# Optimization experiments

Measured on AMD Instinct MI355X. Metric: run time of the kernel, lower is better.

The kernel has to match this reference:

```python
import jax, jax.numpy as jnp
import numpy as np

B, S, D, K = 4, 2048, 1024, 8

def setup_inputs() -> dict:
    key = jax.random.key(0)
    k1, k2, k3 = jax.random.split(key, 3)
    hidden_states = jax.random.normal(k1, (B, S, D), dtype=jnp.float32)
    # scaled so scores ~ O(1) and exp() does not overflow
    W_phi = jax.random.normal(k2, (D, D), dtype=jnp.float32) * 0.005
    W_psi = jax.random.normal(k3, (D, D), dtype=jnp.float32) * 0.005
    return {"hidden_states": hidden_states, "W_phi": W_phi, "W_psi": W_psi, "k": K}

def reference(hidden_states, W_phi, W_psi, k):
    b, s, d = hidden_states.shape
    k = min(k, s)
    # nn.Linear(bias=False): y = x @ W.T
    phi_h = hidden_states @ W_phi.T            # [b,s,d]
    psi_h = hidden_states @ W_psi.T            # [b,s,d]
    scores = jnp.einsum('bsd,btd->bst', phi_h, psi_h)  # [b,s,s]
    affinity = jnp.exp(scores)
    topk_values, topk_indices = jax.lax.top_k(affinity, k)   # [b,s,k]
    norm_sum = topk_values.sum(axis=-1, keepdims=True) + 1e-8
    normalized_weights = topk_values / norm_sum
    batch_offset = (jnp.arange(b) * s)[:, None, None]        # [b,1,1]
    src_local = jnp.arange(s)[None, :, None]                 # [1,s,1]
    src_global = jnp.broadcast_to(batch_offset + src_local, (b, s, k))
    dst_global = batch_offset + topk_indices
    mask = (topk_indices != src_local).reshape(-1)           # drop self-loops
    # eager boolean compaction (data-dependent size, like the torch module)
    src_final = src_global.reshape(-1)[mask]
    dst_final = dst_global.reshape(-1)[mask]
    weights_final = normalized_weights.reshape(-1)[mask]
    if src_final.size == 0:
        all_nodes = jnp.arange(b * s)
        return jnp.stack([all_nodes, all_nodes], axis=0), jnp.ones(b * s, dtype=jnp.float32)
    edge_index = jnp.stack([src_final, dst_final], axis=0)
    return edge_index, weights_final
```

## Files before the change

kernel.cpp:

```cpp
#include <hip/hip_runtime.h>
#include <cmath>

#define SEQ 2048
#define DDIM 1024
#define NROWS 8192
#define KSEL 8
#define NCAND 12
#define IMAXC 0x7fffffff

typedef __attribute__((ext_vector_type(8))) short bf16x8;
typedef __attribute__((ext_vector_type(4))) float f32x4;
typedef __attribute__((ext_vector_type(4))) double f64x4;

__device__ __forceinline__ unsigned short f2bf(float f) {
  unsigned u = __builtin_bit_cast(unsigned, f);
  u = (u + 0x7fffu + ((u >> 16) & 1u)) >> 16;
  return (unsigned short)u;
}
__device__ __forceinline__ float bf2f(unsigned short h) {
  unsigned u = ((unsigned)h) << 16;
  return __builtin_bit_cast(float, u);
}
__device__ __forceinline__ unsigned pkbf(float a, float b) {
  unsigned r;
  asm("v_cvt_pk_bf16_f32 %0, %1, %2" : "=v"(r) : "v"(a), "v"(b));
  return r;
}
__device__ __forceinline__ void dmap(int sel, int lg, int lr, int rg,
                                     int& ri, int& ci) {
  switch (sel) {
    case 0:  ri = (lg << 2) + rg; ci = lr; break;
    case 1:  ri = lg + (rg << 2); ci = lr; break;
    case 2:  ri = lr; ci = (lg << 2) + rg; break;
    default: ri = lr; ci = lg + (rg << 2); break;
  }
}

__global__ void kprobe(int* __restrict__ sel) {
  const int lane = threadIdx.x;
  const int lr = lane & 15, lg = lane >> 4;
  const double a = (double)(4 * lr + lg + 1);
  const double b = (double)(9 * lr + 5 * lg + 2);
  f64x4 d = (f64x4){0.0, 0.0, 0.0, 0.0};
  d = __builtin_amdgcn_mfma_f64_16x16x4f64(a, b, d, 0, 0, 0);
  int my = 4;
  for (int s = 3; s >= 0; --s) {
    bool ok = true;
    for (int rg = 0; rg < 4; ++rg) {
      int ri, ci;
      dmap(s, lg, lr, rg, ri, ci);
      double e = 0.0;
      for (int k = 0; k < 4; ++k)
        e += (double)(4 * ri + k + 1) * (double)(9 * ci + 5 * k + 2);
      ok = ok && (d[rg] == e);
    }
    if (__all(ok)) my = s;
  }
  if (lane == 0) sel[0] = my;
}

#define K0_STAGE(bi)                                        \
  do {                                                      \
    *reinterpret_cast<float4*>(&As[bi][kr][c4]) = pa0;      \
    *reinterpret_cast<float4*>(&As[bi][kr][c4 + 32]) = pa1; \
    *reinterpret_cast<float4*>(&Bs[bi][kr][c4]) = pb0;      \
    *reinterpret_cast<float4*>(&Bs[bi][kr][c4 + 32]) = pb1; \
  } while (0)

__global__ __launch_bounds__(256, 2)
void k0_mfma(const float* __restrict__ A, const float* __restrict__ B,
             float* __restrict__ C, const int* __restrict__ selp) {
  const int sel = selp[0];
  if (sel >= 4) return;
  __shared__ float As[2][32][72];
  __shared__ float Bs[2][32][72];
  const int tid = threadIdx.x;
  const int lane = tid & 63, w = tid >> 6;
  const int wr = w >> 1, wc = w & 1;
  const int lr = lane & 15, lg = lane >> 4;
  const int brow = blockIdx.y << 6, bcol = blockIdx.x << 6;
  const int kr = tid >> 3, c4 = (tid & 7) << 2;

  f64x4 acc[2][2];
#pragma unroll
  for (int mi = 0; mi < 2; ++mi)
#pragma unroll
    for (int nj = 0; nj < 2; ++nj)
      acc[mi][nj] = (f64x4){0.0, 0.0, 0.0, 0.0};

  const float* Ap = &A[(size_t)kr * DDIM + brow + c4];
  const float* Bp = &B[(size_t)kr * DDIM + bcol + c4];
  float4 pa0 = *reinterpret_cast<const float4*>(Ap);
  float4 pa1 = *reinterpret_cast<const float4*>(Ap + 32);
  float4 pb0 = *reinterpret_cast<const float4*>(Bp);
  float4 pb1 = *reinterpret_cast<const float4*>(Bp + 32);
  K0_STAGE(0);
  {
    const size_t nk = (size_t)32 * DDIM;
    pa0 = *reinterpret_cast<const float4*>(Ap + nk);
    pa1 = *reinterpret_cast<const float4*>(Ap + nk + 32);
    pb0 = *reinterpret_cast<const float4*>(Bp + nk);
    pb1 = *reinterpret_cast<const float4*>(Bp + nk + 32);
  }

  for (int t = 0; t < 32; ++t) {
    __syncthreads();
    const int cur = t & 1;
    if (t < 31) {
      K0_STAGE(cur ^ 1);
      if (t < 30) {
        const size_t nk = (size_t)(t + 2) * 32 * DDIM;
        pa0 = *reinterpret_cast<const float4*>(Ap + nk);
        pa1 = *reinterpret_cast<const float4*>(Ap + nk + 32);
        pb0 = *reinterpret_cast<const float4*>(Bp + nk);
        pb1 = *reinterpret_cast<const float4*>(Bp + nk + 32);
      }
    }
    __builtin_amdgcn_s_setprio(1);
#pragma unroll
    for (int kp = 0; kp < 8; ++kp) {
      const int ka = (kp << 2) + lg;
      double a[2], b[2];
#pragma unroll
      for (int mi = 0; mi < 2; ++mi)
        a[mi] = (double)As[cur][ka][(wr << 5) + (mi << 4) + lr];
#pragma unroll
      for (int nj = 0; nj < 2; ++nj)
        b[nj] = (double)Bs[cur][ka][(wc << 5) + (nj << 4) + lr];
#pragma unroll
      for (int mi = 0; mi < 2; ++mi)
#pragma unroll
        for (int nj = 0; nj < 2; ++nj)
          acc[mi][nj] = __builtin_amdgcn_mfma_f64_16x16x4f64(
              a[mi], b[nj], acc[mi][nj], 0, 0, 0);
    }
    __builtin_amdgcn_s_setprio(0);
  }
#pragma unroll
  for (int mi = 0; mi < 2; ++mi)
#pragma unroll
    for (int nj = 0; nj < 2; ++nj)
#pragma unroll
      for (int rg = 0; rg < 4; ++rg) {
        int ri, ci;
        dmap(sel, lg, lr, rg, ri, ci);
        C[(size_t)(brow + (wr << 5) + (mi << 4) + ri) * DDIM +
          bcol + (wc << 5) + (nj << 4) + ci] = (float)acc[mi][nj][rg];
      }
}

__global__ __launch_bounds__(256)
void k0_repair(const float* __restrict__ A, const float* __restrict__ B,
               float* __restrict__ C, const int* __restrict__ selp) {
  if (selp[0] < 4) return;
  __shared__ __align__(16) float As[32][68];
  __shared__ __align__(16) float Bs[32][68];
  const int tid = threadIdx.x;
  const int tx = tid & 15, ty = tid >> 4;
  const int brow = blockIdx.y << 6;
  const int bcol = blockIdx.x << 6;
  double acc[4][4] = {};
  for (int k0 = 0; k0 < DDIM; k0 += 32) {
#pragma unroll
    for (int i = 0; i < 2; ++i) {
      const int f = tid + (i << 8);
      const int r = f >> 4;
      const int c4 = (f & 15) << 2;
      *reinterpret_cast<float4*>(&As[r][c4]) =
          *reinterpret_cast<const float4*>(&A[(size_t)(k0 + r) * DDIM + brow + c4]);
      *reinterpret_cast<float4*>(&Bs[r][c4]) =
          *reinterpret_cast<const float4*>(&B[(size_t)(k0 + r) * DDIM + bcol + c4]);
    }
    __syncthreads();
#pragma unroll
    for (int kk = 0; kk < 32; ++kk) {
      const float4 a = *reinterpret_cast<const float4*>(&As[kk][ty << 2]);
      const float4 b = *reinterpret_cast<const float4*>(&Bs[kk][tx << 2]);
      const double ad[4] = {a.x, a.y, a.z, a.w};
      const double bd[4] = {b.x, b.y, b.z, b.w};
#pragma unroll
      for (int i = 0; i < 4; ++i)
#pragma unroll
        for (int j = 0; j < 4; ++j)
          acc[i][j] = fma(ad[i], bd[j], acc[i][j]);
    }
    __syncthreads();
  }
#pragma unroll
  for (int i = 0; i < 4; ++i) {
    float4 v = make_float4((float)acc[i][0], (float)acc[i][1],
                           (float)acc[i][2], (float)acc[i][3]);
    *reinterpret_cast<float4*>(
        &C[(size_t)(brow + (ty << 2) + i) * DDIM + bcol + (tx << 2)]) = v;
  }
}

#define K1_STAGE(bi)                                                \
  do {                                                              \
    As[bi][akh + 0][ar] = pa0.x;  As[bi][akh + 1][ar] = pa0.y;      \
    As[bi][akh + 2][ar] = pa0.z;  As[bi][akh + 3][ar] = pa0.w;      \
    As[bi][akh + 4][ar] = pa1.x;  As[bi][akh + 5][ar] = pa1.y;      \
    As[bi][akh + 6][ar] = pa1.z;  As[bi][akh + 7][ar] = pa1.w;      \
    As[bi][akh + 16][ar] = pa2.x; As[bi][akh + 17][ar] = pa2.y;     \
    As[bi][akh + 18][ar] = pa2.z; As[bi][akh + 19][ar] = pa2.w;     \
    As[bi][akh + 20][ar] = pa3.x; As[bi][akh + 21][ar] = pa3.y;     \
    As[bi][akh + 22][ar] = pa3.z; As[bi][akh + 23][ar] = pa3.w;     \
    *reinterpret_cast<float4*>(&Bs[bi][bk][bc4]) = pb0;             \
    *reinterpret_cast<float4*>(&Bs[bi][bk][bc4 + 64]) = pb1;        \
    *reinterpret_cast<float4*>(&Bs[bi][bk + 16][bc4]) = pb2;        \
    *reinterpret_cast<float4*>(&Bs[bi][bk + 16][bc4 + 64]) = pb3;   \
  } while (0)

#define K1_LOAD(koff)                                                        \
  do {                                                                       \
    pa0 = *reinterpret_cast<const float4*>(Ap + (koff));                     \
    pa1 = *reinterpret_cast<const float4*>(Ap + (koff) + 4);                 \
    pa2 = *reinterpret_cast<const float4*>(Ap + (koff) + 16);                \
    pa3 = *reinterpret_cast<const float4*>(Ap + (koff) + 20);                \
    pb0 = *reinterpret_cast<const float4*>(Bp + (size_t)(koff) * DDIM);      \
    pb1 = *reinterpret_cast<const float4*>(Bp + (size_t)(koff) * DDIM + 64); \
    pb2 = *reinterpret_cast<const float4*>(Bp + (size_t)((koff) + 16) * DDIM);      \
    pb3 = *reinterpret_cast<const float4*>(Bp + (size_t)((koff) + 16) * DDIM + 64); \
  } while (0)

__global__ __launch_bounds__(256, 2)
void k1_mfma(const float* __restrict__ A, const float* __restrict__ B,
             float* __restrict__ C, const int* __restrict__ selp) {
  const int sel = selp[0];
  if (sel >= 4) return;
  __shared__ float As[2][32][144];
  __shared__ float Bs[2][32][144];
  const int tid = threadIdx.x;
  const int lin = blockIdx.y * 8 + blockIdx.x;
  const int nlin = (lin & 7) * 64 + (lin >> 3);
  const int brow = (nlin >> 3) << 7;
  const int bcol = (nlin & 7) << 7;
  const int lane = tid & 63, w = tid >> 6;
  const int wr = w >> 1, wc = w & 1;
  const int lr = lane & 15, lg = lane >> 4;
  const int ar = tid >> 1, akh = (tid & 1) << 3;
  const int bk = tid >> 4, bc4 = (tid & 15) << 2;

  f64x4 acc[4][4];
#pragma unroll
  for (int mi = 0; mi < 4; ++mi)
#pragma unroll
    for (int nj = 0; nj < 4; ++nj)
      acc[mi][nj] = (f64x4){0.0, 0.0, 0.0, 0.0};

  const float* Ap = &A[(size_t)(brow + ar) * DDIM + akh];
  const float* Bp = &B[(size_t)bk * DDIM + bcol + bc4];

  float4 pa0, pa1, pa2, pa3, pb0, pb1, pb2, pb3;
  K1_LOAD(0);
  K1_STAGE(0);
  K1_LOAD(32);

  for (int t = 0; t < 32; ++t) {
    __syncthreads();
    const int cur = t & 1;
    if (t < 31) {
      K1_STAGE(cur ^ 1);
      if (t < 30) K1_LOAD((size_t)(t + 2) << 5);
    }
    __builtin_amdgcn_s_setprio(1);
#pragma unroll
    for (int kp = 0; kp < 8; ++kp) {
      const int ka = (kp << 2) + lg;
      double a[4], b[4];
#pragma unroll
      for (int mi = 0; mi < 4; ++mi)
        a[mi] = (double)As[cur][ka][(wr << 6) + (mi << 4) + lr];
#pragma unroll
      for (int nj = 0; nj < 4; ++nj)
        b[nj] = (double)Bs[cur][ka][(wc << 6) + (nj << 4) + lr];
#pragma unroll
      for (int mi = 0; mi < 4; ++mi)
#pragma unroll
        for (int nj = 0; nj < 4; ++nj)
          acc[mi][nj] = __builtin_amdgcn_mfma_f64_16x16x4f64(
              a[mi], b[nj], acc[mi][nj], 0, 0, 0);
    }
    __builtin_amdgcn_s_setprio(0);
  }
#pragma unroll
  for (int mi = 0; mi < 4; ++mi)
#pragma unroll
    for (int nj = 0; nj < 4; ++nj)
#pragma unroll
      for (int rg = 0; rg < 4; ++rg) {
        int ri, ci;
        dmap(sel, lg, lr, rg, ri, ci);
        C[(size_t)(brow + (wr << 6) + (mi << 4) + ri) * DDIM +
          bcol + (wc << 6) + (nj << 4) + ci] = (float)acc[mi][nj][rg];
      }
}

__global__ __launch_bounds__(256, 2)
void k1_repair(const float* __restrict__ A, const float* __restrict__ B,
               float* __restrict__ C, const int* __restrict__ selp) {
  if (selp[0] < 4) return;
  __shared__ double As[128][17];
  __shared__ double Bs[16][130];
  const int tid = threadIdx.x;
  const int lin = blockIdx.y * 8 + blockIdx.x;
  const int nlin = (lin & 7) * 64 + (lin >> 3);
  const int brow = (nlin >> 3) << 7;
  const int bcol = (nlin & 7) << 7;
  const int tx = tid & 15, ty = tid >> 4;
  const int ar = tid >> 1, aks = (tid & 1) << 3;
  const int bk = tid >> 4, btx = tid & 15;

  double acc[8][8];
#pragma unroll
  for (int i = 0; i < 8; ++i)
#pragma unroll
    for (int j = 0; j < 8; ++j) acc[i][j] = 0.0;

  const float* Aptr = &A[(size_t)(brow + ar) * DDIM + aks];
  const float* Bptr = &B[(size_t)bk * DDIM + bcol + (btx << 1)];

  float4 pa0, pa1;
  float2 pb[4];
  pa0 = *reinterpret_cast<const float4*>(Aptr);
  pa1 = *reinterpret_cast<const float4*>(Aptr + 4);
#pragma unroll
  for (int w = 0; w < 4; ++w)
    pb[w] = *reinterpret_cast<const float2*>(Bptr + (w << 5));

  for (int k0 = 0; k0 < DDIM; k0 += 16) {
    __syncthreads();
    As[ar][aks + 0] = (double)pa0.x; As[ar][aks + 1] = (double)pa0.y;
    As[ar][aks + 2] = (double)pa0.z; As[ar][aks + 3] = (double)pa0.w;
    As[ar][aks + 4] = (double)pa1.x; As[ar][aks + 5] = (double)pa1.y;
    As[ar][aks + 6] = (double)pa1.z; As[ar][aks + 7] = (double)pa1.w;
#pragma unroll
    for (int w = 0; w < 4; ++w) {
      Bs[bk][(btx << 1) + (w << 5) + 0] = (double)pb[w].x;
      Bs[bk][(btx << 1) + (w << 5) + 1] = (double)pb[w].y;
    }
    __syncthreads();
    if (k0 + 16 < DDIM) {
      pa0 = *reinterpret_cast<const float4*>(Aptr + k0 + 16);
      pa1 = *reinterpret_cast<const float4*>(Aptr + k0 + 20);
#pragma unroll
      for (int w = 0; w < 4; ++w)
        pb[w] = *reinterpret_cast<const float2*>(
            Bptr + (size_t)(k0 + 16) * DDIM + (w << 5));
    }
#pragma unroll 8
    for (int kk = 0; kk < 16; ++kk) {
      double a[8];
      double2 b[4];
#pragma unroll
      for (int i = 0; i < 8; ++i) a[i] = As[(ty << 3) + i][kk];
#pragma unroll
      for (int jj = 0; jj < 4; ++jj)
        b[jj] = *reinterpret_cast<const double2*>(&Bs[kk][(tx << 1) + (jj << 5)]);
#pragma unroll
      for (int i = 0; i < 8; ++i) {
#pragma unroll
        for (int jj = 0; jj < 4; ++jj) {
          acc[i][(jj << 1) + 0] = fma(a[i], b[jj].x, acc[i][(jj << 1) + 0]);
          acc[i][(jj << 1) + 1] = fma(a[i], b[jj].y, acc[i][(jj << 1) + 1]);
        }
      }
    }
  }
#pragma unroll
  for (int i = 0; i < 8; ++i) {
    float* crow = &C[(size_t)(brow + (ty << 3) + i) * DDIM + bcol + (tx << 1)];
#pragma unroll
    for (int jj = 0; jj < 4; ++jj) {
      float2 v = make_float2((float)acc[i][(jj << 1)],
                             (float)acc[i][(jj << 1) + 1]);
      *reinterpret_cast<float2*>(crow + (jj << 5)) = v;
    }
  }
}

#define K2_LOAD(koff)                                                         \
  do {                                                                        \
    _Pragma("unroll")                                                         \
    for (int q = 0; q < 4; ++q) {                                             \
      const int c = (q << 9) + tid;                                           \
      const int row = c >> 3;                                                 \
      const int gs = (c & 7) ^ (row & 7);                                     \
      const float* sT = &T[(size_t)(row0g + row) * DDIM + (koff) + (gs << 3)];\
      rT[2 * q] = *reinterpret_cast<const float4*>(sT);                       \
      rT[2 * q + 1] = *reinterpret_cast<const float4*>(sT + 4);               \
      const float* sH = &H[(size_t)(col0g + row) * DDIM + (koff) + (gs << 3)];\
      rH[2 * q] = *reinterpret_cast<const float4*>(sH);                       \
      rH[2 * q + 1] = *reinterpret_cast<const float4*>(sH + 4);               \
    }                                                                         \
  } while (0)

#define K2_STAGE(bi)                                                          \
  do {                                                                        \
    _Pragma("unroll")                                                         \
    for (int q = 0; q < 4; ++q) {                                             \
      const int c = (q << 9) + tid;                                           \
      uint4 o;                                                                \
      o.x = pkbf(rT[2 * q].x, rT[2 * q].y);                                   \
      o.y = pkbf(rT[2 * q].z, rT[2 * q].w);                                   \
      o.z = pkbf(rT[2 * q + 1].x, rT[2 * q + 1].y);                           \
      o.w = pkbf(rT[2 * q + 1].z, rT[2 * q + 1].w);                           \
      *reinterpret_cast<uint4*>(&u.stage[bi][0][c << 3]) = o;                 \
      uint4 o2;                                                               \
      o2.x = pkbf(rH[2 * q].x, rH[2 * q].y);                                  \
      o2.y = pkbf(rH[2 * q].z, rH[2 * q].w);                                  \
      o2.z = pkbf(rH[2 * q + 1].x, rH[2 * q + 1].y);                          \
      o2.w = pkbf(rH[2 * q + 1].z, rH[2 * q + 1].w);                          \
      *reinterpret_cast<uint4*>(&u.stage[bi][1][c << 3]) = o2;                \
    }                                                                         \
  } while (0)

__global__ __launch_bounds__(512, 1)
void k2_mfma(const float* __restrict__ T, const float* __restrict__ H,
             unsigned short* __restrict__ cand_v,
             unsigned char* __restrict__ cand_i) {
  __shared__ union {
    unsigned short stage[2][2][256 * 64];
    float Sl[64][264];
    struct {
      float mv[512][8];
      unsigned char mi[512][8];
    } mg;
  } u;
  const int tid = threadIdx.x;
  const int lane = tid & 63;
  const int w = tid >> 6;
  const int wr = w >> 2, wc = w & 3;
  const int lr = lane & 15, lg = lane >> 4;
  const int lin = blockIdx.z * 64 + blockIdx.y * 8 + blockIdx.x;
  const int nl = (lin & 7) * 32 + (lin >> 3);
  const int bx = nl & 7;
  const int by = (nl >> 3) & 7;
  const int z = nl >> 6;
  const int brow = by << 8, bcol = bx << 8;
  const int row0g = z * SEQ + brow;
  const int col0g = z * SEQ + bcol;

  f32x4 acc[8][4];
#pragma unroll
  for (int mi = 0; mi < 8; ++mi)
#pragma unroll
    for (int nj = 0; nj < 4; ++nj)
      acc[mi][nj] = (f32x4){0.f, 0.f, 0.f, 0.f};

  float4 rT[8], rH[8];
  K2_LOAD(0);
  K2_STAGE(0);
  K2_LOAD(64);

  for (int t = 0; t < 16; ++t) {
    __syncthreads();
    const int cur = t & 1;
    if (t < 15) {
      K2_STAGE(cur ^ 1);
      if (t < 14) K2_LOAD((t + 2) << 6);
    }
#pragma unroll
    for (int kh2 = 0; kh2 < 2; ++kh2) {
      const int sl = (kh2 << 2) + lg;
      bf16x8 bfv[4];
#pragma unroll
      for (int nj = 0; nj < 4; ++nj) {
        const int rb = (wc << 6) + (nj << 4) + lr;
        bfv[nj] = *reinterpret_cast<const bf16x8*>(
            &u.stage[cur][1][(rb << 6) + ((sl ^ (rb & 7)) << 3)]);
      }
#pragma unroll
      for (int mi = 0; mi < 8; ++mi) {
        const int ra = (wr << 7) + (mi << 4) + lr;
        const bf16x8 af = *reinterpret_cast<const bf16x8*>(
            &u.stage[cur][0][(ra << 6) + ((sl ^ (ra & 7)) << 3)]);
#pragma unroll
        for (int nj = 0; nj < 4; ++nj)
          acc[mi][nj] = __builtin_amdgcn_mfma_f32_16x16x32_bf16(
              af, bfv[nj], acc[mi][nj], 0, 0, 0);
      }
    }
  }

  const int srow = tid >> 3;
  const int qd = tid & 7;
#pragma unroll
  for (int p = 0; p < 4; ++p) {
    __syncthreads();
    if (wr == (p >> 1)) {
      const int mib = (p & 1) << 2;
#pragma unroll
      for (int mi2 = 0; mi2 < 4; ++mi2)
#pragma unroll
        for (int nj = 0; nj < 4; ++nj)
#pragma unroll
          for (int rg = 0; rg < 4; ++rg)
            u.Sl[(mi2 << 4) + (lg << 2) + rg][(wc << 6) + (nj << 4) + lr] =
                acc[mib + mi2][nj][rg];
    }
    __syncthreads();
    float v[KSEL];
    int ci[KSEL];
#pragma unroll
    for (int s = 0; s < KSEL; ++s) { v[s] = -3.0e38f; ci[s] = 0; }
    const int c0 = qd << 5;
    for (int c = 0; c < 32; ++c) {
      const float x = u.Sl[srow][c0 + c];
      if (x > v[KSEL - 1]) {
        float pv = x; int pc = c0 + c;
#pragma unroll
        for (int s = 0; s < KSEL; ++s) {
          if (x > v[s]) {
            const float tv = v[s]; const int tc = ci[s];
            v[s] = pv; ci[s] = pc; pv = tv; pc = tc;
          }
        }
      }
    }
    __syncthreads();
#pragma unroll
    for (int s = 0; s < KSEL; ++s) {
      u.mg.mv[tid][s] = v[s];
      u.mg.mi[tid][s] = (unsigned char)ci[s];
    }
    __syncthreads();
    if (qd == 0) {
      float fv[KSEL];
      int fi[KSEL];
#pragma unroll
      for (int s = 0; s < KSEL; ++s) { fv[s] = -3.0e38f; fi[s] = 0; }
#pragma unroll
      for (int t2 = 0; t2 < 8; ++t2) {
#pragma unroll
        for (int s = 0; s < KSEL; ++s) {
          const float x = u.mg.mv[tid + t2][s];
          const int idx = u.mg.mi[tid + t2][s];
          if (x > fv[KSEL - 1]) {
            float pv = x; int pc = idx;
#pragma unroll
            for (int s2 = 0; s2 < KSEL; ++s2) {
              if (x > fv[s2]) {
                const float tv = fv[s2]; const int tc = fi[s2];
                fv[s2] = pv; fi[s2] = pc; pv = tv; pc = tc;
              }
            }
          }
        }
      }
      const size_t base =
          (size_t)(row0g + (p << 6) + srow) * 64 + ((size_t)bx << 3);
#pragma unroll
      for (int s = 0; s < KSEL; ++s) {
        cand_v[base + s] = f2bf(fv[s]);
        cand_i[base + s] = (unsigned char)fi[s];
      }
    }
  }
}

__global__ __launch_bounds__(256)
void kr_rescore(const float* __restrict__ T, const float* __restrict__ H,
                const unsigned short* __restrict__ cand_v,
                const unsigned char* __restrict__ cand_i,
                int* __restrict__ topi, float* __restrict__ topw,
                int* __restrict__ cnt) {
  __shared__ float smv[2][2][KSEL];
  __shared__ int smi[2][2][KSEL];
  const int tid = threadIdx.x, lane = tid & 63, w = tid >> 6;
  const int rl = w >> 1;
  const int half = w & 1;
  const int r = blockIdx.x * 2 + rl;
  const int b = r >> 11, iloc = r & (SEQ - 1);

  const size_t cbase = (size_t)r * 64;
  float v0 = bf2f(cand_v[cbase + lane]);
  int i0 = ((lane >> 3) << 8) + cand_i[cbase + lane];
  int keep = 0;
  for (int rnd = 0; rnd < NCAND; ++rnd) {
    float m = v0;
#pragma unroll
    for (int off = 32; off >= 1; off >>= 1) m = fmaxf(m, __shfl_xor(m, off));
    const unsigned long long bm = __ballot(v0 == m);
    const int owner = __ffsll(bm) - 1;
    const int oi = __shfl(i0, owner);
    if (lane == owner) v0 = -3.0e38f;
    if (lane == rnd) keep = oi;
  }

  const float* Trow = T + (size_t)r * DDIM;
  float4 t4[4];
#pragma unroll
  for (int q = 0; q < 4; ++q)
    t4[q] = *reinterpret_cast<const float4*>(&Trow[(q << 8) + (lane << 2)]);

  float t8v[KSEL];
  int t8i[KSEL];
#pragma unroll
  for (int p = 0; p < KSEL; ++p) { t8v[p] = -1.0f; t8i[p] = IMAXC; }

  const int c0 = half * (NCAND / 2);
  for (int c = c0; c < c0 + NCAND / 2; ++c) {
    const int j = __shfl(keep, c);
    const float* Hrow = H + ((size_t)(b << 11) + j) * DDIM;
    double s = 0.0;
#pragma unroll
    for (int q = 0; q < 4; ++q) {
      const float4 h = *reinterpret_cast<const float4*>(&Hrow[(q << 8) + (lane << 2)]);
      s = fma((double)t4[q].x, (double)h.x, s);
      s = fma((double)t4[q].y, (double)h.y, s);
      s = fma((double)t4[q].z, (double)h.z, s);
      s = fma((double)t4[q].w, (double)h.w, s);
    }
#pragma unroll
    for (int off = 1; off < 64; off <<= 1) s += __shfl_xor(s, off);
    const float aff = expf((float)s);
    const bool g7 = (aff > t8v[KSEL - 1]) ||
                    (aff == t8v[KSEL - 1] && j < t8i[KSEL - 1]);
    if (g7) {
      float pv = aff; int pi = j;
#pragma unroll
      for (int p = 0; p < KSEL; ++p) {
        const bool g = (aff > t8v[p]) || (aff == t8v[p] && j < t8i[p]);
        if (g) {
          const float tv = t8v[p]; const int ti = t8i[p];
          t8v[p] = pv; t8i[p] = pi; pv = tv; pi = ti;
        }
      }
    }
  }

  if (lane == 0) {
#pragma unroll
    for (int p = 0; p < KSEL; ++p) {
      smv[rl][half][p] = t8v[p];
      smi[rl][half][p] = t8i[p];
    }
  }
  __syncthreads();
  if (half == 0 && lane == 0) {
#pragma unroll
    for (int p = 0; p < KSEL; ++p) {
      const float x = smv[rl][1][p];
      const int jx = smi[rl][1][p];
      const bool g7 = (x > t8v[KSEL - 1]) ||
                      (x == t8v[KSEL - 1] && jx < t8i[KSEL - 1]);
      if (g7) {
        float pv = x; int pi = jx;
#pragma unroll
        for (int q = 0; q < KSEL; ++q) {
          const bool g = (x > t8v[q]) || (x == t8v[q] && jx < t8i[q]);
          if (g) {
            const float tv = t8v[q]; const int ti = t8i[q];
            t8v[q] = pv; t8i[q] = pi; pv = tv; pi = ti;
          }
        }
      }
    }
    float sum = 0.0f;
#pragma unroll
    for (int p = 0; p < KSEL; ++p) sum += t8v[p];
    sum += 1e-8f;
    int c8 = KSEL;
#pragma unroll
    for (int p = 0; p < KSEL; ++p)
      if (t8i[p] == iloc) --c8;
    cnt[r] = c8;
#pragma unroll
    for (int p = 0; p < KSEL; ++p) {
      topi[(size_t)r * KSEL + p] = t8i[p];
      topw[(size_t)r * KSEL + p] = t8v[p] / sum;
    }
  }
}

__global__ __launch_bounds__(1024)
void k4_scan(const int* __restrict__ cnt, int* __restrict__ off) {
  __shared__ int part[1024];
  const int t = threadIdx.x;
  int loc[8];
  int s = 0;
#pragma unroll
  for (int i = 0; i < 8; ++i) { loc[i] = s; s += cnt[t * 8 + i]; }
  part[t] = s;
  __syncthreads();
  for (int d = 1; d < 1024; d <<= 1) {
    const int add = (t >= d) ? part[t - d] : 0;
    __syncthreads();
    part[t] += add;
    __syncthreads();
  }
  const int base = (t == 0) ? 0 : part[t - 1];
#pragma unroll
  for (int i = 0; i < 8; ++i) off[t * 8 + i] = base + loc[i];
}

__global__ __launch_bounds__(256)
void k5_emit(const int* __restrict__ topi, const float* __restrict__ topw,
             const int* __restrict__ off, float* __restrict__ out, int E) {
  const int r = blockIdx.x * 256 + threadIdx.x;
  if (r >= NROWS) return;
  const int o = off[r];
  const int sloc = r & (SEQ - 1);
  const int bbase = r & ~(SEQ - 1);
  int e = 0;
#pragma unroll
  for (int p = 0; p < KSEL; ++p) {
    const int id = topi[(size_t)r * KSEL + p];
    const float w = topw[(size_t)r * KSEL + p];
    if (id != sloc) {
      const int pos = o + e;
      if (pos < E) {
        out[pos] = (float)r;
        out[(size_t)E + pos] = (float)(bbase + id);
        out[2 * (size_t)E + pos] = w;
      }
      ++e;
    }
  }
}

extern "C" void kernel_launch(void* const* d_in, const int* in_sizes, int n_in,
                              void* d_out, int out_size, void* d_ws,
                              size_t ws_size, hipStream_t stream) {
  const float* H = (const float*)d_in[0];
  const float* Wphi = (const float*)d_in[1];
  const float* Wpsi = (const float*)d_in[2];
  float* out = (float*)d_out;
  const int E = out_size / 3;

  char* base = (char*)d_ws;
  float* T = (float*)base;
  char* regionX = base + 33554432;
  float* Wc = (float*)regionX;
  unsigned short* cand_v = (unsigned short*)regionX;
  unsigned char* cand_i = (unsigned char*)(regionX + 2097152);
  char* pp = regionX + 4194304;
  int* topi = (int*)pp;  pp += 262144;
  float* topw = (float*)pp; pp += 262144;
  int* cnt = (int*)pp;   pp += 32768;
  int* off = (int*)pp;   pp += 32768;
  int* sel = (int*)pp;

  kprobe<<<dim3(1), 64, 0, stream>>>(sel);
  k0_mfma<<<dim3(16, 16), 256, 0, stream>>>(Wphi, Wpsi, Wc, sel);
  k0_repair<<<dim3(16, 16), 256, 0, stream>>>(Wphi, Wpsi, Wc, sel);
  k1_mfma<<<dim3(8, 64), 256, 0, stream>>>(H, Wc, T, sel);
  k1_repair<<<dim3(8, 64), 256, 0, stream>>>(H, Wc, T, sel);
  k2_mfma<<<dim3(8, 8, 4), 512, 0, stream>>>(T, H, cand_v, cand_i);
  kr_rescore<<<dim3(NROWS / 2), 256, 0, stream>>>(T, H, cand_v, cand_i,
                                                  topi, topw, cnt);
  k4_scan<<<dim3(1), 1024, 0, stream>>>(cnt, off);
  k5_emit<<<dim3(NROWS / 256), 256, 0, stream>>>(topi, topw, off, out, E);
}
```

Measured before the change: 549.7 us.

## Split-K the weight-product GEMM and inline the MFMA layout probe

The W_phi^T·W_psi product (k0) is split into four K-chunks across a z grid dimension, so it launches 1024 blocks instead of 256. Each chunk writes FP64 partials to workspace, and a separate reduction kernel sums them into the float Wc. The probe kernel that detects the MFMA output layout is removed, and every kernel now recomputes the probe inline, which drops one launch and a global load. In exchange it adds an extra kernel, about 32 MB of partial-sum traffic, and a workspace-size-dependent fallback path.

```diff
diff --git a/kernel.cpp b/kernel.cpp
--- a/kernel.cpp
+++ b/kernel.cpp
@@ -36,8 +36,8 @@
   }
 }
 
-__global__ void kprobe(int* __restrict__ sel) {
-  const int lane = threadIdx.x;
+__device__ __forceinline__ int probe_sel() {
+  const int lane = threadIdx.x & 63;
   const int lr = lane & 15, lg = lane >> 4;
   const double a = (double)(4 * lr + lg + 1);
   const double b = (double)(9 * lr + 5 * lg + 2);
@@ -56,7 +56,7 @@
     }
     if (__all(ok)) my = s;
   }
-  if (lane == 0) sel[0] = my;
+  return my;
 }
 
 #define K0_STAGE(bi)                                        \
@@ -68,9 +68,106 @@
   } while (0)
 
 __global__ __launch_bounds__(256, 2)
+void k0s_mfma(const float* __restrict__ A, const float* __restrict__ B,
+              double* __restrict__ Wp) {
+  const int sel = probe_sel();
+  if (sel >= 4) return;
+  __shared__ float As[2][32][72];
+  __shared__ float Bs[2][32][72];
+  const int tid = threadIdx.x;
+  const int lane = tid & 63, w = tid >> 6;
+  const int wr = w >> 1, wc = w & 1;
+  const int lr = lane & 15, lg = lane >> 4;
+  const int brow = blockIdx.y << 6, bcol = blockIdx.x << 6;
+  const int z = blockIdx.z;
+  const int kr = tid >> 3, c4 = (tid & 7) << 2;
+
+  f64x4 acc[2][2];
+#pragma unroll
+  for (int mi = 0; mi < 2; ++mi)
+#pragma unroll
+    for (int nj = 0; nj < 2; ++nj)
+      acc[mi][nj] = (f64x4){0.0, 0.0, 0.0, 0.0};
+
+  const float* Ap = &A[(size_t)((z << 8) + kr) * DDIM + brow + c4];
+  const float* Bp = &B[(size_t)((z << 8) + kr) * DDIM + bcol + c4];
+  float4 pa0 = *reinterpret_cast<const float4*>(Ap);
+  float4 pa1 = *reinterpret_cast<const float4*>(Ap + 32);
+  float4 pb0 = *reinterpret_cast<const float4*>(Bp);
+  float4 pb1 = *reinterpret_cast<const float4*>(Bp + 32);
+  K0_STAGE(0);
+  {
+    const size_t nk = (size_t)32 * DDIM;
+    pa0 = *reinterpret_cast<const float4*>(Ap + nk);
+    pa1 = *reinterpret_cast<const float4*>(Ap + nk + 32);
+    pb0 = *reinterpret_cast<const float4*>(Bp + nk);
+    pb1 = *reinterpret_cast<const float4*>(Bp + nk + 32);
+  }
+
+  for (int t = 0; t < 8; ++t) {
+    __syncthreads();
+    const int cur = t & 1;
+    if (t < 7) {
+      K0_STAGE(cur ^ 1);
+      if (t < 6) {
+        const size_t nk = (size_t)(t + 2) * 32 * DDIM;
+        pa0 = *reinterpret_cast<const float4*>(Ap + nk);
+        pa1 = *reinterpret_cast<const float4*>(Ap + nk + 32);
+        pb0 = *reinterpret_cast<const float4*>(Bp + nk);
+        pb1 = *reinterpret_cast<const float4*>(Bp + nk + 32);
+      }
+    }
+    __builtin_amdgcn_s_setprio(1);
+#pragma unroll
+    for (int kp = 0; kp < 8; ++kp) {
+      const int ka = (kp << 2) + lg;
+      double a[2], b[2];
+#pragma unroll
+      for (int mi = 0; mi < 2; ++mi)
+        a[mi] = (double)As[cur][ka][(wr << 5) + (mi << 4) + lr];
+#pragma unroll
+      for (int nj = 0; nj < 2; ++nj)
+        b[nj] = (double)Bs[cur][ka][(wc << 5) + (nj << 4) + lr];
+#pragma unroll
+      for (int mi = 0; mi < 2; ++mi)
+#pragma unroll
+        for (int nj = 0; nj < 2; ++nj)
+          acc[mi][nj] = __builtin_amdgcn_mfma_f64_16x16x4f64(
+              a[mi], b[nj], acc[mi][nj], 0, 0, 0);
+    }
+    __builtin_amdgcn_s_setprio(0);
+  }
+  double* Wpz = Wp + ((size_t)z << 20);
+#pragma unroll
+  for (int mi = 0; mi < 2; ++mi)
+#pragma unroll
+    for (int nj = 0; nj < 2; ++nj)
+#pragma unroll
+      for (int rg = 0; rg < 4; ++rg) {
+        int ri, ci;
+        dmap(sel, lg, lr, rg, ri, ci);
+        Wpz[(size_t)(brow + (wr << 5) + (mi << 4) + ri) * DDIM +
+            bcol + (wc << 5) + (nj << 4) + ci] = acc[mi][nj][rg];
+      }
+}
+
+__global__ __launch_bounds__(256)
+void k0red(const double* __restrict__ Wp, float* __restrict__ Wc) {
+  if (probe_sel() >= 4) return;
+  const size_t i = ((size_t)blockIdx.x * 256 + threadIdx.x) << 1;
+  const double2 s0 = *reinterpret_cast<const double2*>(&Wp[i]);
+  const double2 s1 = *reinterpret_cast<const double2*>(&Wp[(1u << 20) + i]);
+  const double2 s2 = *reinterpret_cast<const double2*>(&Wp[(2u << 20) + i]);
+  const double2 s3 = *reinterpret_cast<const double2*>(&Wp[(3u << 20) + i]);
+  const double a = ((s0.x + s1.x) + s2.x) + s3.x;
+  const double b = ((s0.y + s1.y) + s2.y) + s3.y;
+  *reinterpret_cast<float2*>(&Wc[i]) = make_float2((float)a, (float)b);
+}
+
+__global__ __launch_bounds__(256, 2)
 void k0_mfma(const float* __restrict__ A, const float* __restrict__ B,
-             float* __restrict__ C, const int* __restrict__ selp) {
-  const int sel = selp[0];
+             float* __restrict__ C) {
+  const int sel = probe_sel();
   if (sel >= 4) return;
   __shared__ float As[2][32][72];
   __shared__ float Bs[2][32][72];
@@ -151,8 +248,8 @@
 
 __global__ __launch_bounds__(256)
 void k0_repair(const float* __restrict__ A, const float* __restrict__ B,
-               float* __restrict__ C, const int* __restrict__ selp) {
-  if (selp[0] < 4) return;
+               float* __restrict__ C) {
+  if (probe_sel() < 4) return;
   __shared__ __align__(16) float As[32][68];
   __shared__ __align__(16) float Bs[32][68];
   const int tid = threadIdx.x;
@@ -225,8 +322,8 @@
 
 __global__ __launch_bounds__(256, 2)
 void k1_mfma(const float* __restrict__ A, const float* __restrict__ B,
-             float* __restrict__ C, const int* __restrict__ selp) {
-  const int sel = selp[0];
+             float* __restrict__ C) {
+  const int sel = probe_sel();
   if (sel >= 4) return;
   __shared__ float As[2][32][144];
   __shared__ float Bs[2][32][144];
@@ -298,8 +395,8 @@
 
 __global__ __launch_bounds__(256, 2)
 void k1_repair(const float* __restrict__ A, const float* __restrict__ B,
-               float* __restrict__ C, const int* __restrict__ selp) {
-  if (selp[0] < 4) return;
+               float* __restrict__ C) {
+  if (probe_sel() < 4) return;
   __shared__ double As[128][17];
   __shared__ double Bs[16][130];
   const int tid = threadIdx.x;
@@ -740,13 +837,20 @@
   float* topw = (float*)pp; pp += 262144;
   int* cnt = (int*)pp;   pp += 32768;
   int* off = (int*)pp;   pp += 32768;
-  int* sel = (int*)pp;
-
-  kprobe<<<dim3(1), 64, 0, stream>>>(sel);
-  k0_mfma<<<dim3(16, 16), 256, 0, stream>>>(Wphi, Wpsi, Wc, sel);
-  k0_repair<<<dim3(16, 16), 256, 0, stream>>>(Wphi, Wpsi, Wc, sel);
-  k1_mfma<<<dim3(8, 64), 256, 0, stream>>>(H, Wc, T, sel);
-  k1_repair<<<dim3(8, 64), 256, 0, stream>>>(H, Wc, T, sel);
+
+  double* Wp = (double*)(base + 38338560);
+  const size_t NEED_SPLITK = 71892992;
+  const bool splitk = (ws_size >= NEED_SPLITK);
+
+  if (splitk) {
+    k0s_mfma<<<dim3(16, 16, 4), 256, 0, stream>>>(Wphi, Wpsi, Wp);
+    k0red<<<dim3(2048), 256, 0, stream>>>(Wp, Wc);
+  } else {
+    k0_mfma<<<dim3(16, 16), 256, 0, stream>>>(Wphi, Wpsi, Wc);
+  }
+  k0_repair<<<dim3(16, 16), 256, 0, stream>>>(Wphi, Wpsi, Wc);
+  k1_mfma<<<dim3(8, 64), 256, 0, stream>>>(H, Wc, T);
+  k1_repair<<<dim3(8, 64), 256, 0, stream>>>(H, Wc, T);
   k2_mfma<<<dim3(8, 8, 4), 512, 0, stream>>>(T, H, cand_v, cand_i);
   kr_rescore<<<dim3(NROWS / 2), 256, 0, stream>>>(T, H, cand_v, cand_i,
                                                   topi, topw, cnt);
```

Result: no change. 542.3 us (-1.3%).
